# Kernel tuning notes

Hardware: AMD Instinct MI355X
Metric: run time of the kernel (lower is better)

The kernel has to match this reference:

```python
import jax, jax.numpy as jnp
import numpy as np

N, H, L = 128, 2, 1024  # nodes, heads, sequence (input_dim)


def setup_inputs() -> dict:
    key = jax.random.key(0)
    k1, k2 = jax.random.split(key)
    x = jax.random.normal(k1, (N, H, L), dtype=jnp.float32)
    Amat = jax.random.normal(k2, (N, N), dtype=jnp.float32)
    taus = jnp.ones((N, H), dtype=jnp.float32) * 6.2       # as in __init__
    R0dTaus = jnp.ones((N, H), dtype=jnp.float32) * 1.35   # as in __init__
    return {"x": x, "Amat": Amat, "taus": taus, "R0dTaus": R0dTaus}


def reference(x, Amat, taus, R0dTaus):
    n, h, l = x.shape
    idx = jnp.arange(l)
    mask = (idx[:, None] >= idx[None, :])                      # causal lower-tri
    # temporal lag matrix: mat[i,j] = i-j for j<=i else 0 (matches create_temporal_mat)
    mat = jnp.where(mask, (idx[:, None] - idx[None, :]).astype(jnp.float32), 0.0)
    maskf = mask.astype(jnp.float32)

    tempAmat = Amat.T + jnp.eye(n, dtype=x.dtype)              # (n, n)
    signal = jax.nn.relu(x)                                    # (n, h, l)
    Ss = 1.0 - jnp.cumsum(signal, axis=-1)                     # (n, h, l)

    # IsMat[n,h,i,j] = exp((i-j) * log(1 - 1/tau[n,h])) on the causal band
    decay = jnp.log(1.0 - 1.0 / taus)                          # (n, h)
    IsMat = jnp.exp(mat[None, None] * decay[..., None, None]) * maskf  # (n,h,l,l)
    Is = jnp.einsum('nhij,nhj->nhi', IsMat, signal)            # causal decay matvec

    alpha = 1.0 - jnp.exp(-R0dTaus[..., None] * Is)            # (n, h, l)
    # Alpha[k,h,l] = sum_m tempAmat[m,k] * alpha[m,h,l]  (avoids (n,n,h,l) temp)
    Alpha = jnp.einsum('mk,mhl->khl', tempAmat, alpha)
    predSignal = Alpha * Ss
    return (predSignal, signal, tempAmat.T)
```

## Files before the change

### kernel.cpp

```cpp
#include <hip/hip_runtime.h>
#include <hip/hip_bf16.h>

#define NN 128
#define HH 2
#define LL 1024
#define NH (NN * HH)
#define NHL (NN * HH * LL)
#define COLS (HH * LL)

__global__ __launch_bounds__(256) void row_scan_kernel(
    const float* __restrict__ x, const float* __restrict__ taus,
    const float* __restrict__ r0d, float* __restrict__ out_signal,
    float* __restrict__ ws_alpha, float* __restrict__ ws_ss) {
  const int row = blockIdx.x;
  const int tid = threadIdx.x;
  const int lane = tid & 63;
  const int wave = tid >> 6;

  const float4* xr = (const float4*)(x + (size_t)row * LL);
  float4 v = xr[tid];
  float s0 = fmaxf(v.x, 0.f);
  float s1 = fmaxf(v.y, 0.f);
  float s2 = fmaxf(v.z, 0.f);
  float s3 = fmaxf(v.w, 0.f);

  const float tau = taus[row];
  const float d = 1.f - 1.f / tau;
  const float R0 = r0d[row];

  float c0 = s0, c1 = c0 + s1, c2 = c1 + s2, c3 = c2 + s3;
  float l0 = s0;
  float l1 = fmaf(d, l0, s1);
  float l2 = fmaf(d, l1, s2);
  float l3 = fmaf(d, l2, s3);

  float vs = c3;
  float vi = l3;
  float D = d * d;
  D = D * D;
  float Dp = D;
#pragma unroll
  for (int off = 1; off < 64; off <<= 1) {
    float ps = __shfl_up(vs, off);
    float pi = __shfl_up(vi, off);
    if (lane >= off) {
      vs += ps;
      vi = fmaf(Dp, pi, vi);
    }
    Dp *= Dp;
  }

  __shared__ float tw_s[4];
  __shared__ float tw_i[4];
  if (lane == 63) {
    tw_s[wave] = vs;
    tw_i[wave] = vi;
  }
  __syncthreads();

  float S_in = 0.f, I_in = 0.f;
  for (int u = 0; u < wave; ++u) {
    S_in += tw_s[u];
    I_in = fmaf(I_in, Dp, tw_i[u]);
  }

  float es = __shfl_up(vs, 1);
  float ei = __shfl_up(vi, 1);
  if (lane == 0) {
    es = 0.f;
    ei = 0.f;
  }
  const float exs = S_in + es;
  const float state = fmaf(I_in, exp2f((float)lane * log2f(D)), ei);

  float cum0 = exs + c0, cum1 = exs + c1, cum2 = exs + c2, cum3 = exs + c3;
  float is0 = fmaf(d, state, s0);
  float is1 = fmaf(d, is0, s1);
  float is2 = fmaf(d, is1, s2);
  float is3 = fmaf(d, is2, s3);

  float4 sig = make_float4(s0, s1, s2, s3);
  float4 ss = make_float4(1.f - cum0, 1.f - cum1, 1.f - cum2, 1.f - cum3);
  float4 al = make_float4(1.f - __expf(-R0 * is0), 1.f - __expf(-R0 * is1),
                          1.f - __expf(-R0 * is2), 1.f - __expf(-R0 * is3));

  const size_t base = (size_t)row * LL / 4 + tid;
  ((float4*)(out_signal))[base] = sig;
  ((float4*)(ws_alpha))[base] = al;
  ((float4*)(ws_ss))[base] = ss;
}

__global__ __launch_bounds__(256) void mix_kernel(
    const float* __restrict__ Amat, const float* __restrict__ ws_alpha,
    const float* __restrict__ ws_ss, float* __restrict__ pred,
    float* __restrict__ tmatT) {
  const int bid = blockIdx.x;
  const int tid = threadIdx.x;
  const int rg = bid >> 3;
  const int cg = bid & 7;
  const int col = (cg << 8) + tid;
  const int k0 = __builtin_amdgcn_readfirstlane(rg << 2);

  const float* __restrict__ a0 = Amat + (k0 + 0) * NN;
  const float* __restrict__ a1 = Amat + (k0 + 1) * NN;
  const float* __restrict__ a2 = Amat + (k0 + 2) * NN;
  const float* __restrict__ a3 = Amat + (k0 + 3) * NN;

  float acc0 = ws_alpha[(size_t)(k0 + 0) * COLS + col];
  float acc1 = ws_alpha[(size_t)(k0 + 1) * COLS + col];
  float acc2 = ws_alpha[(size_t)(k0 + 2) * COLS + col];
  float acc3 = ws_alpha[(size_t)(k0 + 3) * COLS + col];

  const float* __restrict__ ac = ws_alpha + col;
#pragma unroll 8
  for (int m = 0; m < NN; ++m) {
    const float av = ac[(size_t)m * COLS];
    acc0 = fmaf(a0[m], av, acc0);
    acc1 = fmaf(a1[m], av, acc1);
    acc2 = fmaf(a2[m], av, acc2);
    acc3 = fmaf(a3[m], av, acc3);
  }

  pred[(size_t)(k0 + 0) * COLS + col] =
      acc0 * ws_ss[(size_t)(k0 + 0) * COLS + col];
  pred[(size_t)(k0 + 1) * COLS + col] =
      acc1 * ws_ss[(size_t)(k0 + 1) * COLS + col];
  pred[(size_t)(k0 + 2) * COLS + col] =
      acc2 * ws_ss[(size_t)(k0 + 2) * COLS + col];
  pred[(size_t)(k0 + 3) * COLS + col] =
      acc3 * ws_ss[(size_t)(k0 + 3) * COLS + col];

  const int fid = bid * 256 + tid;
  if (fid < NN * NN / 4) {
    float4 t = ((const float4*)Amat)[fid];
    const int e = fid << 2;
    if (((e + 0) % (NN + 1)) == 0) t.x += 1.f;
    if (((e + 1) % (NN + 1)) == 0) t.y += 1.f;
    if (((e + 2) % (NN + 1)) == 0) t.z += 1.f;
    if (((e + 3) % (NN + 1)) == 0) t.w += 1.f;
    ((float4*)tmatT)[fid] = t;
  }
}

extern "C" void kernel_launch(void* const* d_in, const int* in_sizes, int n_in,
                              void* d_out, int out_size, void* d_ws,
                              size_t ws_size, hipStream_t stream) {
  const float* x = (const float*)d_in[0];
  const float* Amat = (const float*)d_in[1];
  const float* taus = (const float*)d_in[2];
  const float* r0d = (const float*)d_in[3];

  float* out = (float*)d_out;
  float* out_pred = out;
  float* out_signal = out + NHL;
  float* out_tmatT = out + 2 * NHL;

  float* ws = (float*)d_ws;
  float* ws_alpha = ws;
  float* ws_ss = ws + NHL;

  row_scan_kernel<<<NH, 256, 0, stream>>>(x, taus, r0d, out_signal, ws_alpha,
                                          ws_ss);
  mix_kernel<<<256, 256, 0, stream>>>(Amat, ws_alpha, ws_ss, out_pred,
                                      out_tmatT);
}
```

Measured before the change: 67.94 us.

## Fuse scan and mixing kernels into one cooperative launch with grid sync

```diff
diff --git a/kernel.cpp b/kernel.cpp
--- a/kernel.cpp
+++ b/kernel.cpp
@@ -1,5 +1,7 @@
 #include <hip/hip_runtime.h>
-#include <hip/hip_bf16.h>
+#include <hip/hip_cooperative_groups.h>
+
+namespace cg = cooperative_groups;
 
 #define NN 128
 #define HH 2
@@ -8,137 +10,142 @@
 #define NHL (NN * HH * LL)
 #define COLS (HH * LL)
 
-__global__ __launch_bounds__(256) void row_scan_kernel(
-    const float* __restrict__ x, const float* __restrict__ taus,
-    const float* __restrict__ r0d, float* __restrict__ out_signal,
-    float* __restrict__ ws_alpha, float* __restrict__ ws_ss) {
-  const int row = blockIdx.x;
+__global__ __launch_bounds__(256) void fused_kernel(
+    const float* __restrict__ x, const float* __restrict__ Amat,
+    const float* __restrict__ taus, const float* __restrict__ r0d,
+    float* __restrict__ out_pred, float* __restrict__ out_signal,
+    float* __restrict__ out_tmatT, float* __restrict__ ws_alpha,
+    float* __restrict__ ws_ss) {
+  const int bid = blockIdx.x;
   const int tid = threadIdx.x;
-  const int lane = tid & 63;
-  const int wave = tid >> 6;
 
-  const float4* xr = (const float4*)(x + (size_t)row * LL);
-  float4 v = xr[tid];
-  float s0 = fmaxf(v.x, 0.f);
-  float s1 = fmaxf(v.y, 0.f);
-  float s2 = fmaxf(v.z, 0.f);
-  float s3 = fmaxf(v.w, 0.f);
+  {
+    const int row = bid;
+    const int lane = tid & 63;
+    const int wave = tid >> 6;
 
-  const float tau = taus[row];
-  const float d = 1.f - 1.f / tau;
-  const float R0 = r0d[row];
+    const float4* xr = (const float4*)(x + (size_t)row * LL);
+    float4 v = xr[tid];
+    float s0 = fmaxf(v.x, 0.f);
+    float s1 = fmaxf(v.y, 0.f);
+    float s2 = fmaxf(v.z, 0.f);
+    float s3 = fmaxf(v.w, 0.f);
 
-  float c0 = s0, c1 = c0 + s1, c2 = c1 + s2, c3 = c2 + s3;
-  float l0 = s0;
-  float l1 = fmaf(d, l0, s1);
-  float l2 = fmaf(d, l1, s2);
-  float l3 = fmaf(d, l2, s3);
+    const float tau = taus[row];
+    const float d = 1.f - 1.f / tau;
+    const float R0 = r0d[row];
 
-  float vs = c3;
-  float vi = l3;
-  float D = d * d;
-  D = D * D;
-  float Dp = D;
+    float c0 = s0, c1 = c0 + s1, c2 = c1 + s2, c3 = c2 + s3;
+    float l0 = s0;
+    float l1 = fmaf(d, l0, s1);
+    float l2 = fmaf(d, l1, s2);
+    float l3 = fmaf(d, l2, s3);
+
+    float vs = c3;
+    float vi = l3;
+    float D = d * d;
+    D = D * D;
+    float Dp = D;
 #pragma unroll
-  for (int off = 1; off < 64; off <<= 1) {
-    float ps = __shfl_up(vs, off);
-    float pi = __shfl_up(vi, off);
-    if (lane >= off) {
-      vs += ps;
-      vi = fmaf(Dp, pi, vi);
+    for (int off = 1; off < 64; off <<= 1) {
+      float ps = __shfl_up(vs, off);
+      float pi = __shfl_up(vi, off);
+      if (lane >= off) {
+        vs += ps;
+        vi = fmaf(Dp, pi, vi);
+      }
+      Dp *= Dp;
     }
-    Dp *= Dp;
+
+    __shared__ float tw_s[4];
+    __shared__ float tw_i[4];
+    if (lane == 63) {
+      tw_s[wave] = vs;
+      tw_i[wave] = vi;
+    }
+    __syncthreads();
+
+    float S_in = 0.f, I_in = 0.f;
+    for (int u = 0; u < wave; ++u) {
+      S_in += tw_s[u];
+      I_in = fmaf(I_in, Dp, tw_i[u]);
+    }
+
+    float es = __shfl_up(vs, 1);
+    float ei = __shfl_up(vi, 1);
+    if (lane == 0) {
+      es = 0.f;
+      ei = 0.f;
+    }
+    const float exs = S_in + es;
+    const float state = fmaf(I_in, exp2f((float)lane * log2f(D)), ei);
+
+    float cum0 = exs + c0, cum1 = exs + c1, cum2 = exs + c2, cum3 = exs + c3;
+    float is0 = fmaf(d, state, s0);
+    float is1 = fmaf(d, is0, s1);
+    float is2 = fmaf(d, is1, s2);
+    float is3 = fmaf(d, is2, s3);
+
+    float4 sig = make_float4(s0, s1, s2, s3);
+    float4 ss = make_float4(1.f - cum0, 1.f - cum1, 1.f - cum2, 1.f - cum3);
+    float4 al = make_float4(1.f - __expf(-R0 * is0), 1.f - __expf(-R0 * is1),
+                            1.f - __expf(-R0 * is2), 1.f - __expf(-R0 * is3));
+
+    const size_t base = (size_t)row * LL / 4 + tid;
+    ((float4*)(out_signal))[base] = sig;
+    ((float4*)(ws_alpha))[base] = al;
+    ((float4*)(ws_ss))[base] = ss;
   }
 
-  __shared__ float tw_s[4];
-  __shared__ float tw_i[4];
-  if (lane == 63) {
-    tw_s[wave] = vs;
-    tw_i[wave] = vi;
-  }
-  __syncthreads();
-
-  float S_in = 0.f, I_in = 0.f;
-  for (int u = 0; u < wave; ++u) {
-    S_in += tw_s[u];
-    I_in = fmaf(I_in, Dp, tw_i[u]);
+  {
+    const int fid = bid * 256 + tid;
+    if (fid < NN * NN / 4) {
+      float4 t = ((const float4*)Amat)[fid];
+      const int e = fid << 2;
+      if (((e + 0) % (NN + 1)) == 0) t.x += 1.f;
+      if (((e + 1) % (NN + 1)) == 0) t.y += 1.f;
+      if (((e + 2) % (NN + 1)) == 0) t.z += 1.f;
+      if (((e + 3) % (NN + 1)) == 0) t.w += 1.f;
+      ((float4*)out_tmatT)[fid] = t;
+    }
   }
 
-  float es = __shfl_up(vs, 1);
-  float ei = __shfl_up(vi, 1);
-  if (lane == 0) {
-    es = 0.f;
-    ei = 0.f;
-  }
-  const float exs = S_in + es;
-  const float state = fmaf(I_in, exp2f((float)lane * log2f(D)), ei);
+  cg::this_grid().sync();
 
-  float cum0 = exs + c0, cum1 = exs + c1, cum2 = exs + c2, cum3 = exs + c3;
-  float is0 = fmaf(d, state, s0);
-  float is1 = fmaf(d, is0, s1);
-  float is2 = fmaf(d, is1, s2);
-  float is3 = fmaf(d, is2, s3);
+  {
+    const int rg = bid >> 3;
+    const int cg_ = bid & 7;
+    const int col = (cg_ << 8) + tid;
+    const int k0 = __builtin_amdgcn_readfirstlane(rg << 2);
 
-  float4 sig = make_float4(s0, s1, s2, s3);
-  float4 ss = make_float4(1.f - cum0, 1.f - cum1, 1.f - cum2, 1.f - cum3);
-  float4 al = make_float4(1.f - __expf(-R0 * is0), 1.f - __expf(-R0 * is1),
-                          1.f - __expf(-R0 * is2), 1.f - __expf(-R0 * is3));
+    const float* __restrict__ a0 = Amat + (k0 + 0) * NN;
+    const float* __restrict__ a1 = Amat + (k0 + 1) * NN;
+    const float* __restrict__ a2 = Amat + (k0 + 2) * NN;
+    const float* __restrict__ a3 = Amat + (k0 + 3) * NN;
 
-  const size_t base = (size_t)row * LL / 4 + tid;
-  ((float4*)(out_signal))[base] = sig;
-  ((float4*)(ws_alpha))[base] = al;
-  ((float4*)(ws_ss))[base] = ss;
-}
+    float acc0 = ws_alpha[(size_t)(k0 + 0) * COLS + col];
+    float acc1 = ws_alpha[(size_t)(k0 + 1) * COLS + col];
+    float acc2 = ws_alpha[(size_t)(k0 + 2) * COLS + col];
+    float acc3 = ws_alpha[(size_t)(k0 + 3) * COLS + col];
 
-__global__ __launch_bounds__(256) void mix_kernel(
-    const float* __restrict__ Amat, const float* __restrict__ ws_alpha,
-    const float* __restrict__ ws_ss, float* __restrict__ pred,
-    float* __restrict__ tmatT) {
-  const int bid = blockIdx.x;
-  const int tid = threadIdx.x;
-  const int rg = bid >> 3;
-  const int cg = bid & 7;
-  const int col = (cg << 8) + tid;
-  const int k0 = __builtin_amdgcn_readfirstlane(rg << 2);
+    const float* __restrict__ ac = ws_alpha + col;
+#pragma unroll 8
+    for (int m = 0; m < NN; ++m) {
+      const float av = ac[(size_t)m * COLS];
+      acc0 = fmaf(a0[m], av, acc0);
+      acc1 = fmaf(a1[m], av, acc1);
+      acc2 = fmaf(a2[m], av, acc2);
+      acc3 = fmaf(a3[m], av, acc3);
+    }
 
-  const float* __restrict__ a0 = Amat + (k0 + 0) * NN;
-  const float* __restrict__ a1 = Amat + (k0 + 1) * NN;
-  const float* __restrict__ a2 = Amat + (k0 + 2) * NN;
-  const float* __restrict__ a3 = Amat + (k0 + 3) * NN;
-
-  float acc0 = ws_alpha[(size_t)(k0 + 0) * COLS + col];
-  float acc1 = ws_alpha[(size_t)(k0 + 1) * COLS + col];
-  float acc2 = ws_alpha[(size_t)(k0 + 2) * COLS + col];
-  float acc3 = ws_alpha[(size_t)(k0 + 3) * COLS + col];
-
-  const float* __restrict__ ac = ws_alpha + col;
-#pragma unroll 8
-  for (int m = 0; m < NN; ++m) {
-    const float av = ac[(size_t)m * COLS];
-    acc0 = fmaf(a0[m], av, acc0);
-    acc1 = fmaf(a1[m], av, acc1);
-    acc2 = fmaf(a2[m], av, acc2);
-    acc3 = fmaf(a3[m], av, acc3);
-  }
-
-  pred[(size_t)(k0 + 0) * COLS + col] =
-      acc0 * ws_ss[(size_t)(k0 + 0) * COLS + col];
-  pred[(size_t)(k0 + 1) * COLS + col] =
-      acc1 * ws_ss[(size_t)(k0 + 1) * COLS + col];
-  pred[(size_t)(k0 + 2) * COLS + col] =
-      acc2 * ws_ss[(size_t)(k0 + 2) * COLS + col];
-  pred[(size_t)(k0 + 3) * COLS + col] =
-      acc3 * ws_ss[(size_t)(k0 + 3) * COLS + col];
-
-  const int fid = bid * 256 + tid;
-  if (fid < NN * NN / 4) {
-    float4 t = ((const float4*)Amat)[fid];
-    const int e = fid << 2;
-    if (((e + 0) % (NN + 1)) == 0) t.x += 1.f;
-    if (((e + 1) % (NN + 1)) == 0) t.y += 1.f;
-    if (((e + 2) % (NN + 1)) == 0) t.z += 1.f;
-    if (((e + 3) % (NN + 1)) == 0) t.w += 1.f;
-    ((float4*)tmatT)[fid] = t;
+    out_pred[(size_t)(k0 + 0) * COLS + col] =
+        acc0 * ws_ss[(size_t)(k0 + 0) * COLS + col];
+    out_pred[(size_t)(k0 + 1) * COLS + col] =
+        acc1 * ws_ss[(size_t)(k0 + 1) * COLS + col];
+    out_pred[(size_t)(k0 + 2) * COLS + col] =
+        acc2 * ws_ss[(size_t)(k0 + 2) * COLS + col];
+    out_pred[(size_t)(k0 + 3) * COLS + col] =
+        acc3 * ws_ss[(size_t)(k0 + 3) * COLS + col];
   }
 }
 
@@ -159,8 +166,9 @@
   float* ws_alpha = ws;
   float* ws_ss = ws + NHL;
 
-  row_scan_kernel<<<NH, 256, 0, stream>>>(x, taus, r0d, out_signal, ws_alpha,
-                                          ws_ss);
-  mix_kernel<<<256, 256, 0, stream>>>(Amat, ws_alpha, ws_ss, out_pred,
-                                      out_tmatT);
+  void* args[] = {(void*)&x,        (void*)&Amat,       (void*)&taus,
+                  (void*)&r0d,      (void*)&out_pred,   (void*)&out_signal,
+                  (void*)&out_tmatT, (void*)&ws_alpha,  (void*)&ws_ss};
+  hipLaunchCooperativeKernel((const void*)fused_kernel, dim3(NH), dim3(256),
+                             args, 0, stream);
 }
```

Result: slower. 104.2 us (+53.4%).
